# Kernel optimization log

Hardware: AMD Instinct MI355X
Metric: run time of the kernel (lower is better)

## Reference

```python
import jax, jax.numpy as jnp
import numpy as np

BATCH = 16384
MODEL_DIM = 768
SAE_HIDDEN = 16384
K = 3


def setup_inputs() -> dict:
    key = jax.random.key(0)
    k1, k2, k3, k4, k5 = jax.random.split(key, 5)
    scale_enc = 1.0 / np.sqrt(MODEL_DIM)
    scale_dec = 1.0 / np.sqrt(SAE_HIDDEN)
    return {
        "model_activations": jax.random.normal(k1, (BATCH, MODEL_DIM), jnp.float32),
        "W_enc": jax.random.normal(k2, (SAE_HIDDEN, MODEL_DIM), jnp.float32) * scale_enc,
        "b_enc": jax.random.normal(k3, (SAE_HIDDEN,), jnp.float32) * scale_enc,
        "W_dec": jax.random.normal(k4, (MODEL_DIM, SAE_HIDDEN), jnp.float32) * scale_dec,
        "b_dec": jax.random.normal(k5, (MODEL_DIM,), jnp.float32) * scale_dec,
    }


def reference(model_activations, W_enc, b_enc, W_dec, b_dec):
    # encoder linear: [B, D] @ [D, H] + [H] -> [B, H]
    pre_activations = model_activations @ W_enc.T + b_enc
    # top-k (k=3) per row
    topk_vals, topk_idx = jax.lax.top_k(pre_activations, K)  # [B, K]
    # scatter the k values into a zero tensor (sparse activation)
    B = pre_activations.shape[0]
    rows = jnp.arange(B)[:, None]  # [B, 1]
    sae_activations = jnp.zeros_like(pre_activations).at[rows, topk_idx].set(topk_vals)
    # number of unique live latents across the whole batch (static-shape version of torch.unique)
    live_mask = jnp.zeros((pre_activations.shape[1],), dtype=jnp.bool_).at[topk_idx.reshape(-1)].set(True)
    num_live_latents = jnp.sum(live_mask.astype(jnp.int32))
    # decoder linear: [B, H] @ [H, D] + [D] -> [B, D]
    reconstructed = sae_activations @ W_dec.T + b_dec
    return reconstructed, num_live_latents
```

## Files before the change

kernel.cpp:

```cpp
#include <hip/hip_runtime.h>
#include <cstdint>
#include <cstddef>

#define B_ROWS 16384
#define DIM    768
#define HID    16384
#define BM     256
#define BK     64
#define KT_N   (DIM / BK)
#define NCB    (HID / BM)

typedef __bf16 bf16x8 __attribute__((ext_vector_type(8)));
typedef float  f32x4  __attribute__((ext_vector_type(4)));
typedef unsigned int   u32;
typedef unsigned short u16;

__device__ __forceinline__ u32 umaxu(u32 a, u32 b) { return a > b ? a : b; }
__device__ __forceinline__ u32 uminu(u32 a, u32 b) { return a < b ? a : b; }

__device__ __forceinline__ u16 f2bf(float f) {
    u32 u = __float_as_uint(f);
    return (u16)((u + 0x7FFFu + ((u >> 16) & 1u)) >> 16);
}

__device__ __forceinline__ u32 pk(float v, int gidx) {
    u32 b = __float_as_uint(v);
    u32 t = b >> 16;
    t ^= (b & 0x80000000u) ? 0xFFFFu : 0x8000u;
    return (t << 16) | (u32)gidx;
}

__device__ __forceinline__ void gll16(const void* g, void* l) {
    __builtin_amdgcn_global_load_lds(
        (const __attribute__((address_space(1))) unsigned int*)g,
        (__attribute__((address_space(3))) unsigned int*)l, 16, 0, 0);
}

__device__ __forceinline__ void merge3(u32& z0, u32& z1, u32& z2,
                                       u32 A0, u32 A1, u32 A2,
                                       u32 B0, u32 B1, u32 B2) {
    const u32 P = uminu(A0, B0), Q = umaxu(A1, B1);
    const u32 R = uminu(A1, B1), S = umaxu(A2, B2);
    z0 = umaxu(A0, B0);
    z1 = umaxu(P, Q);
    z2 = umaxu(umaxu(uminu(P, Q), R), S);
}

__device__ __forceinline__ bool better(float v1, int i1, float v2, int i2) {
    return (v1 > v2) || (v1 == v2 && i1 < i2);
}
__device__ __forceinline__ void ins3(float v, int i,
                                     float& v0, int& i0, float& v1, int& i1,
                                     float& v2, int& i2) {
    if (better(v, i, v2, i2)) {
        v2 = v; i2 = i;
        if (better(v2, i2, v1, i1)) { float tv = v1; int ti = i1; v1 = v2; i1 = i2; v2 = tv; i2 = ti; }
        if (better(v1, i1, v0, i0)) { float tv = v0; int ti = i0; v0 = v1; i0 = i1; v1 = tv; i1 = ti; }
    }
}

__global__ __launch_bounds__(256) void cast_bf16(const float* __restrict__ X,
                                                 const float* __restrict__ W,
                                                 u16* __restrict__ Xb, u16* __restrict__ Wb) {
    const int n4 = (B_ROWS * DIM) / 4;
    for (int i = blockIdx.x * blockDim.x + threadIdx.x; i < n4; i += gridDim.x * blockDim.x) {
        float4 x = ((const float4*)X)[i];
        float4 w = ((const float4*)W)[i];
        ushort4 xo, wo;
        xo.x = f2bf(x.x); xo.y = f2bf(x.y); xo.z = f2bf(x.z); xo.w = f2bf(x.w);
        wo.x = f2bf(w.x); wo.y = f2bf(w.y); wo.z = f2bf(w.z); wo.w = f2bf(w.w);
        ((ushort4*)Xb)[i] = xo;
        ((ushort4*)Wb)[i] = wo;
    }
}

__global__ __launch_bounds__(512, 2) void gemm_screen(const u16* __restrict__ Xb,
                                                      const u16* __restrict__ Wb,
                                                      const float* __restrict__ benc,
                                                      u32* __restrict__ pvpi) {
    __shared__ __align__(16) u16 As[2 * BM * BK];
    __shared__ __align__(16) u16 Bs[2 * BM * BK];

    const int bid = blockIdx.x;
    const int wg = ((bid & 7) << 9) | (bid >> 3);
    const int st = wg >> 8, loc = wg & 255;
    const int rb = ((st >> 2) << 4) | (loc >> 4);
    const int cb = ((st & 3) << 4) | (loc & 15);
    const int rowBase = rb * BM, colBase = cb * BM;

    const int tid = threadIdx.x;
    const int wid = tid >> 6, lane = tid & 63;
    const int wm = wid >> 2, wn = wid & 3;
    const int j = lane & 15, g = lane >> 4;
    const int js = j & 7;

    const int sr = tid >> 3, ss = tid & 7;
    const int sc = ss ^ (sr & 7);
    const u32 aoff = (u32)(rowBase + sr) * DIM + (u32)sc * 8;
    const u32 boff = (u32)(colBase + sr) * DIM + (u32)sc * 8;
    const int lbw = wid * 512;

#define STAGE_A(H, KTL, D1) do { \
    gll16(Xb + aoff + (H) * 98304u + (u32)(KTL) * 64u,           As + (D1) * 16384 + (H) * 8192 + lbw); \
    gll16(Xb + aoff + (H) * 98304u + 49152u + (u32)(KTL) * 64u,  As + (D1) * 16384 + (H) * 8192 + 4096 + lbw); \
} while (0)
#define STAGE_B(H, KTL, D1) do { \
    gll16(Wb + boff + (H) * 98304u + (u32)(KTL) * 64u,           Bs + (D1) * 16384 + (H) * 8192 + lbw); \
    gll16(Wb + boff + (H) * 98304u + 49152u + (u32)(KTL) * 64u,  Bs + (D1) * 16384 + (H) * 8192 + 4096 + lbw); \
} while (0)

    const bf16x8* As8 = (const bf16x8*)As;
    const bf16x8* Bs8 = (const bf16x8*)Bs;

#define READ_A(MH, D) do { \
    _Pragma("unroll") for (int mtl = 0; mtl < 4; ++mtl) { \
        const int m8_ = (D) * 2048 + (wm * 128 + ((MH) * 4 + mtl) * 16 + j) * 8; \
        aF[mtl][0] = As8[m8_ + ((0 + g) ^ js)]; \
        aF[mtl][1] = As8[m8_ + ((4 + g) ^ js)]; \
    } } while (0)
#define READ_B(DST, NH, D) do { \
    _Pragma("unroll") for (int ntl = 0; ntl < 2; ++ntl) { \
        const int n8_ = (D) * 2048 + (wn * 64 + ((NH) * 2 + ntl) * 16 + j) * 8; \
        DST[ntl][0] = Bs8[n8_ + ((0 + g) ^ js)]; \
        DST[ntl][1] = Bs8[n8_ + ((4 + g) ^ js)]; \
    } } while (0)

#define MFMA_Q(MH, NH, BF) do { \
    __builtin_amdgcn_s_setprio(1); \
    _Pragma("unroll") for (int kk2 = 0; kk2 < 2; ++kk2) \
    _Pragma("unroll") for (int mtl = 0; mtl < 4; ++mtl) \
    _Pragma("unroll") for (int ntl = 0; ntl < 2; ++ntl) \
        acc[(MH) * 4 + mtl][(NH) * 2 + ntl] = __builtin_amdgcn_mfma_f32_16x16x32_bf16( \
            BF[ntl][kk2], aF[mtl][kk2], acc[(MH) * 4 + mtl][(NH) * 2 + ntl], 0, 0, 0); \
    __builtin_amdgcn_s_setprio(0); \
} while (0)

    f32x4 acc[8][4];
#pragma unroll
    for (int mt = 0; mt < 8; ++mt)
#pragma unroll
        for (int nt = 0; nt < 4; ++nt) acc[mt][nt] = (f32x4){0.f, 0.f, 0.f, 0.f};

    STAGE_A(0, 0, 0); STAGE_B(0, 0, 0); STAGE_B(1, 0, 0); STAGE_A(1, 0, 0);
    asm volatile("s_waitcnt vmcnt(4)" ::: "memory");
    __builtin_amdgcn_s_barrier();

    bf16x8 aF[4][2], bLo[2][2], bHi[2][2];

#pragma unroll 1
    for (int t = 0; t < KT_N; ++t) {
        const int d = t & 1, d1 = d ^ 1;
        const bool stg = (t + 1 < KT_N);
        const int kt = t + 1;

        if (stg) { STAGE_A(0, kt, d1); STAGE_B(0, kt, d1); }
        READ_A(0, d);
        READ_B(bLo, 0, d);
        __builtin_amdgcn_s_barrier();
        MFMA_Q(0, 0, bLo);
        if (stg) asm volatile("s_waitcnt vmcnt(6)" ::: "memory");
        else     asm volatile("s_waitcnt vmcnt(2)" ::: "memory");
        __builtin_amdgcn_s_barrier();

        if (stg) STAGE_B(1, kt, d1);
        READ_B(bHi, 1, d);
        __builtin_amdgcn_s_barrier();
        MFMA_Q(0, 1, bHi);
        if (stg) asm volatile("s_waitcnt vmcnt(6)" ::: "memory");
        else     asm volatile("s_waitcnt vmcnt(0)" ::: "memory");
        __builtin_amdgcn_s_barrier();

        if (stg) STAGE_A(1, kt, d1);
        READ_A(1, d);
        __builtin_amdgcn_s_barrier();
        MFMA_Q(1, 1, bHi);
        MFMA_Q(1, 0, bLo);
        if (stg) asm volatile("s_waitcnt vmcnt(4)" ::: "memory");
        __builtin_amdgcn_s_barrier();
    }

    __syncthreads();
    u32* sm = (u32*)As;

    float bias[4][4];
#pragma unroll
    for (int nt = 0; nt < 4; ++nt) {
        const float4 b4 = *(const float4*)(benc + colBase + wn * 64 + nt * 16 + g * 4);
        bias[nt][0] = b4.x; bias[nt][1] = b4.y; bias[nt][2] = b4.z; bias[nt][3] = b4.w;
    }
    const int cb0 = colBase + wn * 64 + g * 4;

#pragma unroll
    for (int mt = 0; mt < 8; ++mt) {
        u32 x0 = 0, x1 = 0, x2 = 0;
#pragma unroll
        for (int nt = 0; nt < 4; ++nt) {
#pragma unroll
            for (int reg = 0; reg < 4; ++reg) {
                const u32 k = pk(acc[mt][nt][reg] + bias[nt][reg], cb0 + nt * 16 + reg);
                const u32 t1 = uminu(x0, k), t2 = uminu(x1, k);
                x0 = umaxu(x0, k); x1 = umaxu(x1, t1); x2 = umaxu(x2, t2);
            }
        }
#pragma unroll
        for (int mk = 16; mk <= 32; mk <<= 1) {
            const u32 y0 = (u32)__shfl_xor((int)x0, mk, 64);
            const u32 y1 = (u32)__shfl_xor((int)x1, mk, 64);
            const u32 y2 = (u32)__shfl_xor((int)x2, mk, 64);
            u32 z0, z1, z2;
            merge3(z0, z1, z2, x0, x1, x2, y0, y1, y2);
            x0 = z0; x1 = z1; x2 = z2;
        }
        if (lane < 16) {
            const int row = wm * 128 + mt * 16 + j;
            sm[row * 12 + wn * 3 + 0] = x0;
            sm[row * 12 + wn * 3 + 1] = x1;
            sm[row * 12 + wn * 3 + 2] = x2;
        }
    }
    __syncthreads();
    if (tid < 256) {
        const int row = tid;
        const u32* s = sm + row * 12;
        u32 m0, m1, m2, n0, n1, n2, z0, z1, z2;
        merge3(m0, m1, m2, s[0], s[1], s[2], s[3], s[4], s[5]);
        merge3(n0, n1, n2, s[6], s[7], s[8], s[9], s[10], s[11]);
        merge3(z0, z1, z2, m0, m1, m2, n0, n1, n2);
        const size_t base = ((size_t)(rowBase + row) * NCB + cb) * 3;
        pvpi[base + 0] = z0; pvpi[base + 1] = z1; pvpi[base + 2] = z2;
    }
#undef STAGE_A
#undef STAGE_B
#undef READ_A
#undef READ_B
#undef MFMA_Q
}

__global__ __launch_bounds__(256) void reduce_recheck(
        const u32* __restrict__ pvpi, const float* __restrict__ X,
        const float* __restrict__ Wenc, const float* __restrict__ benc,
        float* __restrict__ fv, int* __restrict__ fi, int* __restrict__ mask) {
    const int wid = threadIdx.x >> 6, lane = threadIdx.x & 63;
    const int row = blockIdx.x * 4 + wid;

    const u32* p = pvpi + (size_t)row * (NCB * 3);
    u32 k[3];
#pragma unroll
    for (int t = 0; t < 3; t++) k[t] = p[t * 64 + lane];

    u32 cand[16];
#pragma unroll
    for (int it = 0; it < 16; ++it) {
        u32 m = umaxu(umaxu(k[0], k[1]), k[2]);
#pragma unroll
        for (int mk = 1; mk < 64; mk <<= 1) m = umaxu(m, (u32)__shfl_xor((int)m, mk, 64));
        cand[it] = m;
#pragma unroll
        for (int t = 0; t < 3; t++) if (k[t] == m) k[t] = 0;
    }

    const float4* xp = (const float4*)(X + (size_t)row * DIM) + lane * 3;
    const float4 x0 = xp[0], x1 = xp[1], x2 = xp[2];

    float v0 = -INFINITY, v1 = -INFINITY, v2 = -INFINITY;
    int   i0 = 0x7fffffff, i1 = 0x7fffffff, i2 = 0x7fffffff;
#pragma unroll
    for (int it = 0; it < 16; ++it) {
        const int ci = (int)(cand[it] & 0xFFFFu);
        const float4* wq = (const float4*)(Wenc + (size_t)ci * DIM) + lane * 3;
        const float4 w0 = wq[0], w1 = wq[1], w2 = wq[2];
        float s = x0.x * w0.x;
        s = fmaf(x0.y, w0.y, s); s = fmaf(x0.z, w0.z, s); s = fmaf(x0.w, w0.w, s);
        s = fmaf(x1.x, w1.x, s); s = fmaf(x1.y, w1.y, s); s = fmaf(x1.z, w1.z, s);
        s = fmaf(x1.w, w1.w, s); s = fmaf(x2.x, w2.x, s); s = fmaf(x2.y, w2.y, s);
        s = fmaf(x2.z, w2.z, s); s = fmaf(x2.w, w2.w, s);
#pragma unroll
        for (int mk = 1; mk < 64; mk <<= 1) s += __shfl_xor(s, mk, 64);
        const float val = s + benc[ci];
        ins3(val, ci, v0, i0, v1, i1, v2, i2);
    }
    if (lane == 0) {
        fv[row * 3 + 0] = v0; fv[row * 3 + 1] = v1; fv[row * 3 + 2] = v2;
        fi[row * 3 + 0] = i0; fi[row * 3 + 1] = i1; fi[row * 3 + 2] = i2;
        mask[i0] = 1; mask[i1] = 1; mask[i2] = 1;
    }
}

__global__ __launch_bounds__(256) void count_live(const int* __restrict__ mask,
                                                  float* __restrict__ outScalar) {
    __shared__ int sd[256];
    const int tid = threadIdx.x;
    int s = 0;
    for (int i = tid; i < HID; i += 256) s += mask[i];
    sd[tid] = s;
    __syncthreads();
    for (int st = 128; st > 0; st >>= 1) {
        if (tid < st) sd[tid] += sd[tid + st];
        __syncthreads();
    }
    if (tid == 0) outScalar[0] = (float)sd[0];
}

__global__ __launch_bounds__(256) void transpose_wdec(const float* __restrict__ W,
                                                      float* __restrict__ Wt) {
    __shared__ float t[32][33];
    const int bx = blockIdx.x;
    const int by = blockIdx.y;
    const int x = threadIdx.x & 31;
    const int y = threadIdx.x >> 5;
#pragma unroll
    for (int i = 0; i < 4; i++) {
        const int d = by * 32 + y + i * 8;
        t[y + i * 8][x] = W[(size_t)d * HID + bx * 32 + x];
    }
    __syncthreads();
#pragma unroll
    for (int i = 0; i < 4; i++) {
        const int h = bx * 32 + y + i * 8;
        Wt[(size_t)h * DIM + by * 32 + x] = t[x][y + i * 8];
    }
}

__global__ __launch_bounds__(192) void decode_rows(
        const float* __restrict__ fv, const int* __restrict__ fi,
        const float* __restrict__ Wt, const float* __restrict__ bdec,
        float* __restrict__ out) {
    const int row = blockIdx.x;
    const int tid = threadIdx.x;
    const float v0 = fv[row * 3 + 0], v1 = fv[row * 3 + 1], v2 = fv[row * 3 + 2];
    const int   i0 = fi[row * 3 + 0], i1 = fi[row * 3 + 1], i2 = fi[row * 3 + 2];
    const int jj = tid * 4;
    const float4 b  = *(const float4*)(bdec + jj);
    const float4 w0 = *(const float4*)(Wt + (size_t)i0 * DIM + jj);
    const float4 w1 = *(const float4*)(Wt + (size_t)i1 * DIM + jj);
    const float4 w2 = *(const float4*)(Wt + (size_t)i2 * DIM + jj);
    float4 o;
    o.x = b.x + v0 * w0.x + v1 * w1.x + v2 * w2.x;
    o.y = b.y + v0 * w0.y + v1 * w1.y + v2 * w2.y;
    o.z = b.z + v0 * w0.z + v1 * w1.z + v2 * w2.z;
    o.w = b.w + v0 * w0.w + v1 * w1.w + v2 * w2.w;
    *(float4*)(out + (size_t)row * DIM + jj) = o;
}

extern "C" void kernel_launch(void* const* d_in, const int* in_sizes, int n_in,
                              void* d_out, int out_size, void* d_ws, size_t ws_size,
                              hipStream_t stream) {
    const float* X    = (const float*)d_in[0];
    const float* Wenc = (const float*)d_in[1];
    const float* benc = (const float*)d_in[2];
    const float* Wdec = (const float*)d_in[3];
    const float* bdec = (const float*)d_in[4];
    float* out = (float*)d_out;

    char* ws = (char*)d_ws;
    u16*   Xb   = (u16*)ws;
    u16*   Wb   = (u16*)(ws + 25165824);
    float* Wt   = (float*)ws;
    u32*   pvpi = (u32*)(ws + 50331648);
    float* fv   = (float*)(ws + 62914560);
    int*   fi   = (int*)(ws + 63111168);
    int*   mask = (int*)(ws + 63307776);

    hipMemsetAsync(mask, 0, HID * sizeof(int), stream);

    cast_bf16<<<3072, 256, 0, stream>>>(X, Wenc, Xb, Wb);
    gemm_screen<<<4096, 512, 0, stream>>>(Xb, Wb, benc, pvpi);
    reduce_recheck<<<B_ROWS / 4, 256, 0, stream>>>(pvpi, X, Wenc, benc, fv, fi, mask);
    count_live<<<1, 256, 0, stream>>>(mask, out + (size_t)B_ROWS * DIM);
    transpose_wdec<<<dim3(HID / 32, DIM / 32), 256, 0, stream>>>(Wdec, Wt);
    decode_rows<<<B_ROWS, 192, 0, stream>>>(fv, fi, Wt, bdec, out);
}
```

Before: 973.5 us.

## Rework encoder GEMM main loop into a 4-stage ring with BK=32

The screening GEMM drops its double-buffered BK=64 loop, which interleaved half-tile loads, reads and MFMA quarters across six barriers per step. It now uses a 4-slot ring of BK=32 tiles with three stages in flight and a single barrier per k-step. The LDS layout is re-swizzled so each 64-element line packs two rows of 32 k-values, and all A and B fragments for a step are loaded before one block of 32 MFMAs. The aim is to cut barrier overhead and hide more global-load latency. The cost is twice as many loop iterations and more live fragment registers per step, which may add register pressure under the 2-blocks-per-CU launch bound.

```diff
diff --git a/kernel.cpp b/kernel.cpp
--- a/kernel.cpp
+++ b/kernel.cpp
@@ -6,8 +6,8 @@
 #define DIM    768
 #define HID    16384
 #define BM     256
-#define BK     64
-#define KT_N   (DIM / BK)
+#define BK     32
+#define KT     (DIM / BK)
 #define NCB    (HID / BM)
 
 typedef __bf16 bf16x8 __attribute__((ext_vector_type(8)));
@@ -78,62 +78,50 @@
                                                       const u16* __restrict__ Wb,
                                                       const float* __restrict__ benc,
                                                       u32* __restrict__ pvpi) {
-    __shared__ __align__(16) u16 As[2 * BM * BK];
-    __shared__ __align__(16) u16 Bs[2 * BM * BK];
+    __shared__ __align__(16) u16 As[4 * BM * BK];
+    __shared__ __align__(16) u16 Bs[4 * BM * BK];
 
     const int bid = blockIdx.x;
     const int wg = ((bid & 7) << 9) | (bid >> 3);
     const int st = wg >> 8, loc = wg & 255;
     const int rb = ((st >> 2) << 4) | (loc >> 4);
-    const int cb = ((st & 3) << 4) | (loc & 15);
-    const int rowBase = rb * BM, colBase = cb * BM;
+    const int cbk = ((st & 3) << 4) | (loc & 15);
+    const int rowBase = rb * BM, colBase = cbk * BM;
 
     const int tid = threadIdx.x;
     const int wid = tid >> 6, lane = tid & 63;
     const int wm = wid >> 2, wn = wid & 3;
     const int j = lane & 15, g = lane >> 4;
-    const int js = j & 7;
-
-    const int sr = tid >> 3, ss = tid & 7;
-    const int sc = ss ^ (sr & 7);
-    const u32 aoff = (u32)(rowBase + sr) * DIM + (u32)sc * 8;
-    const u32 boff = (u32)(colBase + sr) * DIM + (u32)sc * 8;
+
+    u32 srcA[2], srcB[2];
+#pragma unroll
+    for (int q = 0; q < 2; ++q) {
+        const int p = q * 512 + tid;
+        const int line = p >> 3, slot = p & 7;
+        const int c = slot ^ (line & 7);
+        const int row = (line << 1) | (c >> 2);
+        const int gc = c & 3;
+        srcA[q] = (u32)(rowBase + row) * DIM + (u32)gc * 8;
+        srcB[q] = (u32)(colBase + row) * DIM + (u32)gc * 8;
+    }
     const int lbw = wid * 512;
 
-#define STAGE_A(H, KTL, D1) do { \
-    gll16(Xb + aoff + (H) * 98304u + (u32)(KTL) * 64u,           As + (D1) * 16384 + (H) * 8192 + lbw); \
-    gll16(Xb + aoff + (H) * 98304u + 49152u + (u32)(KTL) * 64u,  As + (D1) * 16384 + (H) * 8192 + 4096 + lbw); \
+#define STAGE(T) do { \
+    const int rb_ = ((T) & 3) * 8192; \
+    const u32 ko_ = (u32)(T) * 32u; \
+    gll16(Xb + srcA[0] + ko_, As + rb_ + lbw); \
+    gll16(Xb + srcA[1] + ko_, As + rb_ + 4096 + lbw); \
+    gll16(Wb + srcB[0] + ko_, Bs + rb_ + lbw); \
+    gll16(Wb + srcB[1] + ko_, Bs + rb_ + 4096 + lbw); \
 } while (0)
-#define STAGE_B(H, KTL, D1) do { \
-    gll16(Wb + boff + (H) * 98304u + (u32)(KTL) * 64u,           Bs + (D1) * 16384 + (H) * 8192 + lbw); \
-    gll16(Wb + boff + (H) * 98304u + 49152u + (u32)(KTL) * 64u,  Bs + (D1) * 16384 + (H) * 8192 + 4096 + lbw); \
-} while (0)
-
-    const bf16x8* As8 = (const bf16x8*)As;
-    const bf16x8* Bs8 = (const bf16x8*)Bs;
-
-#define READ_A(MH, D) do { \
-    _Pragma("unroll") for (int mtl = 0; mtl < 4; ++mtl) { \
-        const int m8_ = (D) * 2048 + (wm * 128 + ((MH) * 4 + mtl) * 16 + j) * 8; \
-        aF[mtl][0] = As8[m8_ + ((0 + g) ^ js)]; \
-        aF[mtl][1] = As8[m8_ + ((4 + g) ^ js)]; \
-    } } while (0)
-#define READ_B(DST, NH, D) do { \
-    _Pragma("unroll") for (int ntl = 0; ntl < 2; ++ntl) { \
-        const int n8_ = (D) * 2048 + (wn * 64 + ((NH) * 2 + ntl) * 16 + j) * 8; \
-        DST[ntl][0] = Bs8[n8_ + ((0 + g) ^ js)]; \
-        DST[ntl][1] = Bs8[n8_ + ((4 + g) ^ js)]; \
-    } } while (0)
-
-#define MFMA_Q(MH, NH, BF) do { \
-    __builtin_amdgcn_s_setprio(1); \
-    _Pragma("unroll") for (int kk2 = 0; kk2 < 2; ++kk2) \
-    _Pragma("unroll") for (int mtl = 0; mtl < 4; ++mtl) \
-    _Pragma("unroll") for (int ntl = 0; ntl < 2; ++ntl) \
-        acc[(MH) * 4 + mtl][(NH) * 2 + ntl] = __builtin_amdgcn_mfma_f32_16x16x32_bf16( \
-            BF[ntl][kk2], aF[mtl][kk2], acc[(MH) * 4 + mtl][(NH) * 2 + ntl], 0, 0, 0); \
-    __builtin_amdgcn_s_setprio(0); \
-} while (0)
+
+    const int lh = j >> 1;
+    const int cg = (j & 1) * 4 + g;
+    int aoff[8], boff[4];
+#pragma unroll
+    for (int m = 0; m < 8; ++m) aoff[m] = (wm * 64 + m * 8 + lh) * 8 + (cg ^ lh);
+#pragma unroll
+    for (int n = 0; n < 4; ++n) boff[n] = (wn * 32 + n * 8 + lh) * 8 + (cg ^ lh);
 
     f32x4 acc[8][4];
 #pragma unroll
@@ -141,42 +129,34 @@
 #pragma unroll
         for (int nt = 0; nt < 4; ++nt) acc[mt][nt] = (f32x4){0.f, 0.f, 0.f, 0.f};
 
-    STAGE_A(0, 0, 0); STAGE_B(0, 0, 0); STAGE_B(1, 0, 0); STAGE_A(1, 0, 0);
-    asm volatile("s_waitcnt vmcnt(4)" ::: "memory");
+    STAGE(0); STAGE(1); STAGE(2);
+    asm volatile("s_waitcnt vmcnt(8)" ::: "memory");
     __builtin_amdgcn_s_barrier();
 
-    bf16x8 aF[4][2], bLo[2][2], bHi[2][2];
-
 #pragma unroll 1
-    for (int t = 0; t < KT_N; ++t) {
-        const int d = t & 1, d1 = d ^ 1;
-        const bool stg = (t + 1 < KT_N);
-        const int kt = t + 1;
-
-        if (stg) { STAGE_A(0, kt, d1); STAGE_B(0, kt, d1); }
-        READ_A(0, d);
-        READ_B(bLo, 0, d);
-        __builtin_amdgcn_s_barrier();
-        MFMA_Q(0, 0, bLo);
-        if (stg) asm volatile("s_waitcnt vmcnt(6)" ::: "memory");
-        else     asm volatile("s_waitcnt vmcnt(2)" ::: "memory");
-        __builtin_amdgcn_s_barrier();
-
-        if (stg) STAGE_B(1, kt, d1);
-        READ_B(bHi, 1, d);
-        __builtin_amdgcn_s_barrier();
-        MFMA_Q(0, 1, bHi);
-        if (stg) asm volatile("s_waitcnt vmcnt(6)" ::: "memory");
-        else     asm volatile("s_waitcnt vmcnt(0)" ::: "memory");
-        __builtin_amdgcn_s_barrier();
-
-        if (stg) STAGE_A(1, kt, d1);
-        READ_A(1, d);
-        __builtin_amdgcn_s_barrier();
-        MFMA_Q(1, 1, bHi);
-        MFMA_Q(1, 0, bLo);
-        if (stg) asm volatile("s_waitcnt vmcnt(4)" ::: "memory");
-        __builtin_amdgcn_s_barrier();
+    for (int t = 0; t < KT; ++t) {
+        if (t + 3 < KT) STAGE(t + 3);
+
+        const bf16x8* Ab = (const bf16x8*)As + (t & 3) * 1024;
+        const bf16x8* Bb = (const bf16x8*)Bs + (t & 3) * 1024;
+        bf16x8 bF[4], aF[8];
+#pragma unroll
+        for (int n = 0; n < 4; ++n) bF[n] = Bb[boff[n]];
+#pragma unroll
+        for (int m = 0; m < 8; ++m) aF[m] = Ab[aoff[m]];
+
+        __builtin_amdgcn_s_setprio(1);
+#pragma unroll
+        for (int m = 0; m < 8; ++m)
+#pragma unroll
+            for (int n = 0; n < 4; ++n)
+                acc[m][n] = __builtin_amdgcn_mfma_f32_16x16x32_bf16(bF[n], aF[m], acc[m][n], 0, 0, 0);
+        __builtin_amdgcn_s_setprio(0);
+
+        if (t + 3 < KT)      asm volatile("s_waitcnt vmcnt(8)" ::: "memory");
+        else if (t + 2 < KT) asm volatile("s_waitcnt vmcnt(4)" ::: "memory");
+        else if (t + 1 < KT) asm volatile("s_waitcnt vmcnt(0)" ::: "memory");
+        if (t + 1 < KT) __builtin_amdgcn_s_barrier();
     }
 
     __syncthreads();
@@ -226,14 +206,10 @@
         merge3(m0, m1, m2, s[0], s[1], s[2], s[3], s[4], s[5]);
         merge3(n0, n1, n2, s[6], s[7], s[8], s[9], s[10], s[11]);
         merge3(z0, z1, z2, m0, m1, m2, n0, n1, n2);
-        const size_t base = ((size_t)(rowBase + row) * NCB + cb) * 3;
+        const size_t base = ((size_t)(rowBase + row) * NCB + cbk) * 3;
         pvpi[base + 0] = z0; pvpi[base + 1] = z1; pvpi[base + 2] = z2;
     }
-#undef STAGE_A
-#undef STAGE_B
-#undef READ_A
-#undef READ_B
-#undef MFMA_Q
+#undef STAGE
 }
 
 __global__ __launch_bounds__(256) void reduce_recheck(
```

Result: faster. 879.0 us (-9.7%).
